# Optimization experiments

Hardware: AMD Instinct MI355X
Metric: run time of the kernel (lower is better)

## Reference

```python
import jax, jax.numpy as jnp
import numpy as np
from jax import lax

# ---- model dims (from init_kwargs) ----
H_SIZE = 2048      # hidden_size
NK = 16            # linear_num_key_heads
NV = 32            # linear_num_value_heads
DK = 128           # linear_key_head_dim
DV = 128           # linear_value_head_dim
KCONV = 4          # linear_conv_kernel_dim
KEY_DIM = NK * DK          # 2048
VAL_DIM = NV * DV          # 4096
CONV_DIM = 2 * KEY_DIM + VAL_DIM  # 8192
B, S = 2, 2048
EPS = 1e-6


def _l2norm(x, eps=EPS):
    return x * lax.rsqrt(jnp.sum(x * x, axis=-1, keepdims=True) + eps)


def setup_inputs() -> dict:
    key = jax.random.key(0)
    ks = jax.random.split(key, 7)
    x = jax.random.normal(ks[0], (B, S, H_SIZE), jnp.float32)
    W_qkvz = jax.random.normal(ks[1], (2 * KEY_DIM + 2 * VAL_DIM, H_SIZE), jnp.float32) * 0.02
    W_ba = jax.random.normal(ks[2], (2 * NV, H_SIZE), jnp.float32) * 0.02
    conv_w = jax.random.normal(ks[3], (CONV_DIM, 1, KCONV), jnp.float32) * 0.2  # depthwise OIH
    dt_bias = jnp.ones((NV,), jnp.float32)
    A_log = jnp.log(jax.random.uniform(ks[4], (NV,), jnp.float32, 1e-3, 16.0))
    norm_w = jnp.zeros((VAL_DIM,), jnp.float32)
    W_out = jax.random.normal(ks[5], (H_SIZE, VAL_DIM), jnp.float32) * 0.02
    return {"x": x, "W_qkvz": W_qkvz, "W_ba": W_ba, "conv_w": conv_w,
            "dt_bias": dt_bias, "A_log": A_log, "norm_w": norm_w, "W_out": W_out}


def reference(x, W_qkvz, W_ba, conv_w, dt_bias, A_log, norm_w, W_out):
    bs, s, _ = x.shape
    qkvz = jnp.einsum('bsh,ph->bsp', x, W_qkvz)
    ba = jnp.einsum('bsh,ph->bsp', x, W_ba)
    q, k, v, z = jnp.split(qkvz, [KEY_DIM, 2 * KEY_DIM, 2 * KEY_DIM + VAL_DIM], axis=-1)
    b, a = jnp.split(ba, [NV], axis=-1)

    # causal depthwise conv1d over channels (left pad K-1), then SiLU
    mixed = jnp.concatenate([q, k, v], axis=-1).transpose(0, 2, 1)  # [B, CONV_DIM, S]
    mixed = lax.conv_general_dilated(
        mixed, conv_w, window_strides=(1,), padding=[(KCONV - 1, 0)],
        dimension_numbers=('NCH', 'OIH', 'NCH'), feature_group_count=CONV_DIM)
    mixed = jax.nn.silu(mixed).transpose(0, 2, 1)  # [B, S, CONV_DIM]
    q, k, v = jnp.split(mixed, [KEY_DIM, 2 * KEY_DIM], axis=-1)

    q = q.reshape(bs, s, NK, DK)
    k = k.reshape(bs, s, NK, DK)
    v = v.reshape(bs, s, NV, DV)
    beta = jax.nn.sigmoid(b)                                   # [B,S,NV]
    g = -jnp.exp(A_log) * jax.nn.softplus(a + dt_bias)         # [B,S,NV]

    rep = NV // NK
    if rep > 1:
        q = jnp.repeat(q, rep, axis=2)
        k = jnp.repeat(k, rep, axis=2)
    q = _l2norm(q).astype(jnp.float32)
    k = _l2norm(k).astype(jnp.float32)
    v = v.astype(jnp.float32)

    # time-major for scan: [S, B, H, d]
    qs = q.transpose(1, 0, 2, 3)
    ks_ = k.transpose(1, 0, 2, 3)
    vs = v.transpose(1, 0, 2, 3)
    ge = jnp.exp(g).transpose(1, 0, 2)      # [S,B,H]
    bs_ = beta.astype(jnp.float32).transpose(1, 0, 2)  # [S,B,H]

    state0 = jnp.zeros((bs, NV, DK, DV), jnp.float32)

    def step(state, ts):
        q_t, k_t, v_t, g_t, b_t = ts
        state = state * g_t[..., None, None]
        kv_mem = jnp.einsum('bhk,bhkv->bhv', k_t, state)
        delta = b_t[..., None] * (v_t - kv_mem)
        state = state + jnp.einsum('bhk,bhv->bhkv', k_t, delta)
        o_t = jnp.einsum('bhk,bhkv->bhv', q_t, state)
        return state, o_t

    _, core = lax.scan(step, state0, (qs, ks_, vs, ge, bs_))  # core: [S,B,H,DV]
    core = core.transpose(1, 0, 2, 3).reshape(bs, s, VAL_DIM)

    # RMSNorm with (1 + weight) scale
    core = core * lax.rsqrt(jnp.mean(core * core, axis=-1, keepdims=True) + EPS)
    core = core * (1.0 + norm_w)
    core = core * jax.nn.silu(z)
    return jnp.einsum('bsv,hv->bsh', core, W_out)
```

## Files before the change

### kernel.cpp

```cpp
#include <hip/hip_runtime.h>
#include <hip/hip_bf16.h>
#include <math.h>

#define TOK    4096
#define HS     2048
#define CONVD  8192
#define KEYD   2048
#define VALD   4096
#define NKH    16
#define NVH    32
#define DKH    128
#define DVH    128
#define SEQ    2048
#define NBATCH 2
#define EPSF   1e-6f
#define CHUNK  64
#define NCHUNK 32

typedef __attribute__((ext_vector_type(8))) short short8;
typedef __attribute__((ext_vector_type(4))) float floatx4;

static __device__ __forceinline__ unsigned short f2bf(float x) {
  union { float f; unsigned u; } c; c.f = x;
  unsigned r = (c.u + 0x7FFF + ((c.u >> 16) & 1)) >> 16;
  return (unsigned short)r;
}
static __device__ __forceinline__ float bf2f(unsigned short u) {
  union { unsigned u; float f; } c; c.u = ((unsigned)u) << 16;
  return c.f;
}

#define BAR() do { \
  __builtin_amdgcn_sched_barrier(0); \
  asm volatile("s_waitcnt lgkmcnt(0)" ::: "memory"); \
  __builtin_amdgcn_s_barrier(); \
  __builtin_amdgcn_sched_barrier(0); \
} while (0)

__global__ __launch_bounds__(256) void gemm_nt(
    const float* __restrict__ A, const float* __restrict__ B,
    float* __restrict__ C, int M, int N, int K) {
  __shared__ float As[16][68];
  __shared__ float Bs[16][68];
  const int tx = threadIdx.x & 15;
  const int ty = threadIdx.x >> 4;
  const int row0 = blockIdx.y * 64;
  const int col0 = blockIdx.x * 64;
  const int lr = threadIdx.x >> 2;
  const int lc = (threadIdx.x & 3) * 4;
  float acc[4][4] = {};
  for (int k0 = 0; k0 < K; k0 += 16) {
    float4 av = *(const float4*)&A[(size_t)(row0 + lr) * K + (k0 + lc)];
    float4 bv = *(const float4*)&B[(size_t)(col0 + lr) * K + (k0 + lc)];
    As[lc + 0][lr] = av.x; As[lc + 1][lr] = av.y;
    As[lc + 2][lr] = av.z; As[lc + 3][lr] = av.w;
    Bs[lc + 0][lr] = bv.x; Bs[lc + 1][lr] = bv.y;
    Bs[lc + 2][lr] = bv.z; Bs[lc + 3][lr] = bv.w;
    __syncthreads();
    #pragma unroll
    for (int kk = 0; kk < 16; kk++) {
      float a[4], b[4];
      #pragma unroll
      for (int i = 0; i < 4; i++) a[i] = As[kk][ty * 4 + i];
      #pragma unroll
      for (int i = 0; i < 4; i++) b[i] = Bs[kk][tx * 4 + i];
      #pragma unroll
      for (int i = 0; i < 4; i++)
        #pragma unroll
        for (int j = 0; j < 4; j++)
          acc[i][j] += a[i] * b[j];
    }
    __syncthreads();
  }
  #pragma unroll
  for (int i = 0; i < 4; i++) {
    float4 v = make_float4(acc[i][0], acc[i][1], acc[i][2], acc[i][3]);
    *(float4*)&C[(size_t)(row0 + ty * 4 + i) * N + (col0 + tx * 4)] = v;
  }
}

__global__ __launch_bounds__(256) void cast_bf16(
    const float4* __restrict__ src, ushort4* __restrict__ dst, int n4) {
  int i = blockIdx.x * 256 + threadIdx.x;
  if (i < n4) {
    float4 v = src[i];
    ushort4 o;
    o.x = f2bf(v.x); o.y = f2bf(v.y); o.z = f2bf(v.z); o.w = f2bf(v.w);
    dst[i] = o;
  }
}

__global__ __launch_bounds__(256) void gemm_bf16_nt(
    const ushort* __restrict__ A, const ushort* __restrict__ B,
    float* __restrict__ C, int M, int N, int K) {
  __shared__ ushort Asm[128 * 32];
  __shared__ ushort Bsm[128 * 32];
  const int tid = threadIdx.x;
  const int w = tid >> 6, l = tid & 63;
  const int row0 = blockIdx.y * 128, col0 = blockIdx.x * 128;
  const int wm = w >> 1, wn = w & 1;

  floatx4 acc[4][4];
  #pragma unroll
  for (int i = 0; i < 4; i++)
    #pragma unroll
    for (int j = 0; j < 4; j++)
      acc[i][j] = (floatx4){0.f, 0.f, 0.f, 0.f};

  const int srow = w * 16 + (l >> 2);
  const int scol = (l & 3) * 8;
  const ushort* Ag = A + (size_t)(row0 + srow) * K + scol;
  const ushort* Bg = B + (size_t)(col0 + srow) * K + scol;

  for (int k0 = 0; k0 < K; k0 += 32) {
    #pragma unroll
    for (int c = 0; c < 2; c++) {
      __builtin_amdgcn_global_load_lds(
          (const __attribute__((address_space(1))) void*)(Ag + (size_t)(c * 64) * K + k0),
          (__attribute__((address_space(3))) void*)&Asm[(c * 64 + w * 16) * 32],
          16, 0, 0);
      __builtin_amdgcn_global_load_lds(
          (const __attribute__((address_space(1))) void*)(Bg + (size_t)(c * 64) * K + k0),
          (__attribute__((address_space(3))) void*)&Bsm[(c * 64 + w * 16) * 32],
          16, 0, 0);
    }
    __syncthreads();
    short8 af[4], bfv[4];
    #pragma unroll
    for (int i = 0; i < 4; i++) {
      af[i]  = *(const short8*)&Asm[(wm * 64 + i * 16 + (l & 15)) * 32 + (l >> 4) * 8];
      bfv[i] = *(const short8*)&Bsm[(wn * 64 + i * 16 + (l & 15)) * 32 + (l >> 4) * 8];
    }
    #pragma unroll
    for (int i = 0; i < 4; i++)
      #pragma unroll
      for (int j = 0; j < 4; j++)
        acc[i][j] = __builtin_amdgcn_mfma_f32_16x16x32_bf16(af[i], bfv[j], acc[i][j], 0, 0, 0);
    __syncthreads();
  }

  const int cl = l & 15, rq = l >> 4;
  #pragma unroll
  for (int i = 0; i < 4; i++) {
    int r0 = row0 + wm * 64 + i * 16 + rq * 4;
    #pragma unroll
    for (int j = 0; j < 4; j++) {
      int cc = col0 + wn * 64 + j * 16 + cl;
      #pragma unroll
      for (int r = 0; r < 4; r++)
        C[(size_t)(r0 + r) * N + cc] = acc[i][j][r];
    }
  }
}

__global__ __launch_bounds__(256) void conv_silu(
    const float* __restrict__ qkv, const float* __restrict__ cw,
    float* __restrict__ mix) {
  size_t idx = (size_t)blockIdx.x * 256 + threadIdx.x;
  int c = (int)(idx % CONVD);
  size_t t = idx / CONVD;
  int s = (int)(t % SEQ);
  float w0 = cw[c * 4 + 0], w1 = cw[c * 4 + 1], w2 = cw[c * 4 + 2], w3 = cw[c * 4 + 3];
  const float* col = qkv + t * CONVD + c;
  float acc = w3 * col[0];
  if (s >= 1) acc += w2 * col[-(ptrdiff_t)CONVD];
  if (s >= 2) acc += w1 * col[-2 * (ptrdiff_t)CONVD];
  if (s >= 3) acc += w0 * col[-3 * (ptrdiff_t)CONVD];
  float sig = 1.f / (1.f + expf(-acc));
  mix[t * CONVD + c] = acc * sig;
}

__global__ __launch_bounds__(256) void gates_kernel(
    const float* __restrict__ ba, const float* __restrict__ A_log,
    const float* __restrict__ dt_bias, float2* __restrict__ g2) {
  int idx = blockIdx.x * 256 + threadIdx.x;
  int h = idx & 31;
  size_t t = (size_t)(idx >> 5);
  float bv = ba[t * 64 + h];
  float av = ba[t * 64 + 32 + h];
  float beta = 1.f / (1.f + expf(-bv));
  float xx = av + dt_bias[h];
  float sp = (xx > 20.f) ? xx : log1pf(expf(xx));
  float lg = -expf(A_log[h]) * sp;
  g2[t * 32 + h] = make_float2(lg, beta);
}

__global__ __launch_bounds__(256) void l2norm_qk(
    const float* __restrict__ mix, ushort* __restrict__ kq) {
  int wid = (blockIdx.x * 256 + threadIdx.x) >> 6;
  int lane = threadIdx.x & 63;
  size_t t = (size_t)(wid >> 5);
  int hh = wid & 31;
  const float* p = mix + t * CONVD + (size_t)hh * DKH;
  float v0 = p[lane], v1 = p[lane + 64];
  float ss = v0 * v0 + v1 * v1;
  #pragma unroll
  for (int off = 32; off >= 1; off >>= 1) ss += __shfl_xor(ss, off, 64);
  float sc = rsqrtf(ss + EPSF);
  ushort* q = kq + t * 4096 + (size_t)hh * DKH;
  q[lane] = f2bf(v0 * sc);
  q[lane + 64] = f2bf(v1 * sc);
}

__global__ __launch_bounds__(64) void chunk_prep(
    const ushort* __restrict__ kq, const float2* __restrict__ g2,
    float* __restrict__ Lgbuf, ushort* __restrict__ Tbuf,
    ushort* __restrict__ Mbuf) {
  const int blk = blockIdx.x;
  const int ch = blk & 31;
  const int h  = (blk >> 5) & 31;
  const int b  = blk >> 10;
  const int kh = h >> 1;
  const int l  = threadIdx.x;
  const int fr = l & 15;
  const int fc8 = (l >> 4) * 8;
  const int cr = (l >> 4) * 4;

  __shared__ float sLg[64], sB[64];
  __shared__ float sA[64 * 65];
  __shared__ float sT[64 * 65];

  float2 gv = g2[((size_t)(b * SEQ + ch * 64 + l)) * 32 + h];
  float lg = gv.x;
  #pragma unroll
  for (int off = 1; off < 64; off <<= 1) {
    float n = __shfl_up(lg, off, 64);
    if (l >= off) lg += n;
  }
  sLg[l] = lg; sB[l] = gv.y;
  Lgbuf[(size_t)blk * 64 + l] = lg;
  __syncthreads();

  const ushort* qb = kq + ((size_t)(b * SEQ + ch * 64)) * 4096 + (size_t)kh * DKH;
  const ushort* kb = qb + 2048;

  floatx4 zero4 = {0.f, 0.f, 0.f, 0.f};
  floatx4 kk[4][4], qk[4][4];
  #pragma unroll
  for (int i = 0; i < 4; i++)
    #pragma unroll
    for (int j = 0; j < 4; j++) { kk[i][j] = zero4; qk[i][j] = zero4; }

  for (int ks = 0; ks < 4; ks++) {
    short8 kf[4], qf[4];
    #pragma unroll
    for (int m = 0; m < 4; m++) {
      kf[m] = *(const short8*)(kb + (size_t)(m * 16 + fr) * 4096 + fc8 + ks * 32);
      qf[m] = *(const short8*)(qb + (size_t)(m * 16 + fr) * 4096 + fc8 + ks * 32);
    }
    #pragma unroll
    for (int mt = 0; mt < 4; mt++)
      #pragma unroll
      for (int nt = 0; nt < 4; nt++) {
        kk[mt][nt] = __builtin_amdgcn_mfma_f32_16x16x32_bf16(kf[mt], kf[nt], kk[mt][nt], 0, 0, 0);
        qk[mt][nt] = __builtin_amdgcn_mfma_f32_16x16x32_bf16(qf[mt], kf[nt], qk[mt][nt], 0, 0, 0);
      }
  }

  const size_t tmbase = (size_t)blk * 4096;
  #pragma unroll
  for (int mt = 0; mt < 4; mt++)
    #pragma unroll
    for (int r = 0; r < 4; r++) {
      int i = mt * 16 + cr + r;
      float Li = sLg[i], Bi = sB[i];
      #pragma unroll
      for (int nt = 0; nt < 4; nt++) {
        int j = nt * 16 + fr;
        float dec = expf(Li - sLg[j]);
        sA[i * 65 + j] = (j < i) ? Bi * dec * kk[mt][nt][r] : 0.f;
        float mv = (j <= i) ? dec * qk[mt][nt][r] : 0.f;
        Mbuf[tmbase + (size_t)i * 64 + j] = f2bf(mv);
      }
    }
  __syncthreads();

  sT[0 * 65 + l] = (l == 0) ? 1.f : 0.f;
  for (int i = 1; i < 64; i++) {
    float acc = (l == i) ? 1.f : 0.f;
    for (int j = 0; j < i; j++)
      acc -= sA[i * 65 + j] * sT[j * 65 + l];
    sT[i * 65 + l] = acc;
  }
  for (int i = 0; i < 64; i++)
    Tbuf[tmbase + (size_t)i * 64 + l] = f2bf(sT[i * 65 + l]);
}

struct KReg { short8 K[4]; float gLg, gB, gLgC; };

__global__ __launch_bounds__(256, 1) void chunk_scan(
    const float* __restrict__ mix, const ushort* __restrict__ kq,
    const float2* __restrict__ g2, const float* __restrict__ Lgbuf,
    const ushort* __restrict__ Tbuf, const ushort* __restrict__ Mbuf,
    float* __restrict__ core) {
  const int blk = blockIdx.x;
  const int vq = blk & 3;
  const int bh = blk >> 2;
  const int h = bh & 31;
  const int b = bh >> 5;
  const int kh = h >> 1;
  const int tid = threadIdx.x;
  const int w = tid >> 6;
  const int l = tid & 63;
  const int fr = l & 15;
  const int fc8 = (l >> 4) * 8;
  const int cr = (l >> 4) * 4;
  const int w16 = w * 16, w32 = w * 32;
  const int ia = w16 + fr;

  __shared__ __align__(16) ushort Kt[64][136];
  __shared__ __align__(16) ushort STh[32][136], STl[32][136];
  __shared__ __align__(16) ushort DTh[32][72],  DTl[32][72];
  __shared__ float sKB[64], sQv[64], sKh[64], sBe[64], sLgC[1];

  for (int i = tid; i < 32 * 136; i += 256) { (&STh[0][0])[i] = 0; (&STl[0][0])[i] = 0; }

  floatx4 zero4 = {0.f, 0.f, 0.f, 0.f};
  floatx4 sacc[2][2] = {{zero4, zero4}, {zero4, zero4}};

  const size_t mixb = (size_t)b * SEQ * CONVD;
  const float* vb = mix + mixb + 2 * KEYD + (size_t)h * DVH + vq * 32;
  const ushort* kq_q = kq + (size_t)b * SEQ * 4096 + (size_t)kh * DKH;
  const ushort* kq_k = kq_q + 2048;
  const ushort* Tb = Tbuf + (size_t)bh * 32 * 4096;
  const ushort* Mb = Mbuf + (size_t)bh * 32 * 4096;
  const float* Lgb = Lgbuf + (size_t)bh * 2048;
  const float2* gp = g2 + (size_t)b * SEQ * 32 + h;
  float* cbase = core + (size_t)b * SEQ * VALD + (size_t)h * DVH + vq * 32;

  auto kpre = [&](KReg& R, int ch) {
    size_t ro = (size_t)(ch * 64 + ia) * 4096;
    #pragma unroll
    for (int ks = 0; ks < 4; ks++)
      R.K[ks] = *(const short8*)(kq_k + ro + fc8 + ks * 32);
    if (tid < 64) {
      R.gLg = Lgb[ch * 64 + tid];
      R.gLgC = Lgb[ch * 64 + 63];
      R.gB = gp[(size_t)(ch * 64 + tid) * 32].y;
    }
  };

  auto body = [&](KReg& cur, KReg& nxt, int ch) {
    const int tok0 = ch * 64;
    if (tid < 64) {
      float e = expf(cur.gLg);
      sKB[tid] = cur.gB * e;
      sQv[tid] = e;
      sKh[tid] = expf(cur.gLgC - cur.gLg);
      sBe[tid] = cur.gB;
      if (tid == 0) sLgC[0] = cur.gLgC;
    }
    #pragma unroll
    for (int ks = 0; ks < 4; ks++)
      *(short8*)&Kt[ia][fc8 + ks * 32] = cur.K[ks];
    short8 Qr[4], Tr[2], Mr[2];
    float Vr[8];
    {
      size_t ro = (size_t)(tok0 + ia) * 4096;
      #pragma unroll
      for (int ks = 0; ks < 4; ks++)
        Qr[ks] = *(const short8*)(kq_q + ro + fc8 + ks * 32);
      size_t tmb = (size_t)ch * 4096 + (size_t)ia * 64;
      #pragma unroll
      for (int ks = 0; ks < 2; ks++) {
        Tr[ks] = *(const short8*)(Tb + tmb + fc8 + ks * 32);
        Mr[ks] = *(const short8*)(Mb + tmb + fc8 + ks * 32);
      }
      #pragma unroll
      for (int nt = 0; nt < 2; nt++)
        #pragma unroll
        for (int r = 0; r < 4; r++)
          Vr[nt * 4 + r] = vb[(size_t)(tok0 + w16 + cr + r) * CONVD + nt * 16 + fr];
    }
    BAR();
    kpre(nxt, (ch + 1 < NCHUNK) ? ch + 1 : NCHUNK - 1);

    floatx4 p[2] = {zero4, zero4};
    #pragma unroll
    for (int ks = 0; ks < 4; ks++)
      #pragma unroll
      for (int nt = 0; nt < 2; nt++) {
        short8 bh_ = *(const short8*)&STh[nt * 16 + fr][fc8 + ks * 32];
        short8 bl_ = *(const short8*)&STl[nt * 16 + fr][fc8 + ks * 32];
        p[nt] = __builtin_amdgcn_mfma_f32_16x16x32_bf16(cur.K[ks], bh_, p[nt], 0, 0, 0);
        p[nt] = __builtin_amdgcn_mfma_f32_16x16x32_bf16(cur.K[ks], bl_, p[nt], 0, 0, 0);
      }
    #pragma unroll
    for (int nt = 0; nt < 2; nt++) {
      unsigned hv[4], lv[4];
      #pragma unroll
      for (int r = 0; r < 4; r++) {
        int i = w16 + cr + r;
        float Rv = sBe[i] * Vr[nt * 4 + r] - sKB[i] * p[nt][r];
        unsigned short hq = f2bf(Rv);
        hv[r] = hq; lv[r] = f2bf(Rv - bf2f(hq));
      }
      int v = nt * 16 + fr;
      *(uint2*)&DTh[v][w16 + cr] = make_uint2(hv[0] | (hv[1] << 16), hv[2] | (hv[3] << 16));
      *(uint2*)&DTl[v][w16 + cr] = make_uint2(lv[0] | (lv[1] << 16), lv[2] | (lv[3] << 16));
    }
    BAR();

    floatx4 d[2] = {zero4, zero4};
    #pragma unroll
    for (int ks = 0; ks < 2; ks++)
      #pragma unroll
      for (int nt = 0; nt < 2; nt++) {
        short8 bh_ = *(const short8*)&DTh[nt * 16 + fr][fc8 + ks * 32];
        short8 bl_ = *(const short8*)&DTl[nt * 16 + fr][fc8 + ks * 32];
        d[nt] = __builtin_amdgcn_mfma_f32_16x16x32_bf16(Tr[ks], bh_, d[nt], 0, 0, 0);
        d[nt] = __builtin_amdgcn_mfma_f32_16x16x32_bf16(Tr[ks], bl_, d[nt], 0, 0, 0);
      }
    BAR();
    #pragma unroll
    for (int nt = 0; nt < 2; nt++) {
      unsigned hv[4], lv[4];
      #pragma unroll
      for (int r = 0; r < 4; r++) {
        float dv = d[nt][r];
        unsigned short hq = f2bf(dv);
        hv[r] = hq; lv[r] = f2bf(dv - bf2f(hq));
      }
      int v = nt * 16 + fr;
      *(uint2*)&DTh[v][w16 + cr] = make_uint2(hv[0] | (hv[1] << 16), hv[2] | (hv[3] << 16));
      *(uint2*)&DTl[v][w16 + cr] = make_uint2(lv[0] | (lv[1] << 16), lv[2] | (lv[3] << 16));
    }
    BAR();

    floatx4 oq[2] = {zero4, zero4}, od[2] = {zero4, zero4};
    #pragma unroll
    for (int ks = 0; ks < 4; ks++)
      #pragma unroll
      for (int nt = 0; nt < 2; nt++) {
        short8 bh_ = *(const short8*)&STh[nt * 16 + fr][fc8 + ks * 32];
        short8 bl_ = *(const short8*)&STl[nt * 16 + fr][fc8 + ks * 32];
        oq[nt] = __builtin_amdgcn_mfma_f32_16x16x32_bf16(Qr[ks], bh_, oq[nt], 0, 0, 0);
        oq[nt] = __builtin_amdgcn_mfma_f32_16x16x32_bf16(Qr[ks], bl_, oq[nt], 0, 0, 0);
      }
    #pragma unroll
    for (int ks = 0; ks < 2; ks++)
      #pragma unroll
      for (int nt = 0; nt < 2; nt++) {
        short8 bh_ = *(const short8*)&DTh[nt * 16 + fr][fc8 + ks * 32];
        short8 bl_ = *(const short8*)&DTl[nt * 16 + fr][fc8 + ks * 32];
        od[nt] = __builtin_amdgcn_mfma_f32_16x16x32_bf16(Mr[ks], bh_, od[nt], 0, 0, 0);
        od[nt] = __builtin_amdgcn_mfma_f32_16x16x32_bf16(Mr[ks], bl_, od[nt], 0, 0, 0);
      }
    #pragma unroll
    for (int nt = 0; nt < 2; nt++)
      #pragma unroll
      for (int r = 0; r < 4; r++) {
        int i = w16 + cr + r;
        cbase[(size_t)(tok0 + i) * VALD + nt * 16 + fr] = sQv[i] * oq[nt][r] + od[nt][r];
      }

    float eL = expf(sLgC[0]);
    #pragma unroll
    for (int mt = 0; mt < 2; mt++)
      #pragma unroll
      for (int nt = 0; nt < 2; nt++)
        #pragma unroll
        for (int r = 0; r < 4; r++)
          sacc[mt][nt][r] *= eL;
    #pragma unroll
    for (int ks = 0; ks < 2; ks++) {
      short8 afm[2];
      #pragma unroll
      for (int mt = 0; mt < 2; mt++) {
        short8 a;
        #pragma unroll
        for (int jj = 0; jj < 8; jj++) {
          int tk = fc8 + ks * 32 + jj;
          float kv = bf2f(Kt[tk][w32 + mt * 16 + fr]);
          a[jj] = (short)f2bf(kv * sKh[tk]);
        }
        afm[mt] = a;
      }
      #pragma unroll
      for (int mt = 0; mt < 2; mt++)
        #pragma unroll
        for (int nt = 0; nt < 2; nt++) {
          short8 bh_ = *(const short8*)&DTh[nt * 16 + fr][fc8 + ks * 32];
          short8 bl_ = *(const short8*)&DTl[nt * 16 + fr][fc8 + ks * 32];
          sacc[mt][nt] = __builtin_amdgcn_mfma_f32_16x16x32_bf16(afm[mt], bh_, sacc[mt][nt], 0, 0, 0);
          sacc[mt][nt] = __builtin_amdgcn_mfma_f32_16x16x32_bf16(afm[mt], bl_, sacc[mt][nt], 0, 0, 0);
        }
    }
    BAR();
    #pragma unroll
    for (int mt = 0; mt < 2; mt++)
      #pragma unroll
      for (int nt = 0; nt < 2; nt++) {
        unsigned hv[4], lv[4];
        #pragma unroll
        for (int r = 0; r < 4; r++) {
          float sv = sacc[mt][nt][r];
          unsigned short hq = f2bf(sv);
          hv[r] = hq; lv[r] = f2bf(sv - bf2f(hq));
        }
        int v = nt * 16 + fr, k0 = w32 + mt * 16 + cr;
        *(uint2*)&STh[v][k0] = make_uint2(hv[0] | (hv[1] << 16), hv[2] | (hv[3] << 16));
        *(uint2*)&STl[v][k0] = make_uint2(lv[0] | (lv[1] << 16), lv[2] | (lv[3] << 16));
      }
  };

  KReg RA, RB;
  RA.gLg = RA.gB = RA.gLgC = 0.f;
  RB.gLg = RB.gB = RB.gLgC = 0.f;
  kpre(RA, 0);
  #pragma unroll 1
  for (int ch = 0; ch < NCHUNK; ch += 2) {
    body(RA, RB, ch);
    body(RB, RA, ch + 1);
  }
}

__global__ __launch_bounds__(256) void rmsnorm_silu(
    const float* __restrict__ core, const float* __restrict__ zbuf,
    const float* __restrict__ norm_w, ushort* __restrict__ out_bf) {
  int t = blockIdx.x;
  int tid = threadIdx.x;
  const float* row = core + (size_t)t * VALD;
  const float* zrow = zbuf + (size_t)t * VALD;
  ushort* orow = out_bf + (size_t)t * VALD;
  float vals[16];
  float ss = 0.f;
  #pragma unroll
  for (int i = 0; i < 16; i++) { float x = row[tid + i * 256]; vals[i] = x; ss += x * x; }
  #pragma unroll
  for (int off = 32; off >= 1; off >>= 1) ss += __shfl_xor(ss, off, 64);
  __shared__ float red[4];
  if ((tid & 63) == 0) red[tid >> 6] = ss;
  __syncthreads();
  float tot = red[0] + red[1] + red[2] + red[3];
  float scale = rsqrtf(tot * (1.f / VALD) + EPSF);
  #pragma unroll
  for (int i = 0; i < 16; i++) {
    int c = tid + i * 256;
    float z = zrow[c];
    float sz = z / (1.f + expf(-z));
    orow[c] = f2bf(vals[i] * scale * (1.f + norm_w[c]) * sz);
  }
}

extern "C" void kernel_launch(void* const* d_in, const int* in_sizes, int n_in,
                              void* d_out, int out_size, void* d_ws, size_t ws_size,
                              hipStream_t stream) {
  const float* x       = (const float*)d_in[0];
  const float* W_qkvz  = (const float*)d_in[1];
  const float* W_ba    = (const float*)d_in[2];
  const float* conv_w  = (const float*)d_in[3];
  const float* dt_bias = (const float*)d_in[4];
  const float* A_log   = (const float*)d_in[5];
  const float* norm_w  = (const float*)d_in[6];
  const float* W_out   = (const float*)d_in[7];
  float* out = (float*)d_out;

  float* ws = (float*)d_ws;
  float* A  = ws;
  float* Bp = A + (size_t)33554432;
  float* Cp = Bp + (size_t)33554432;
  float* ba = Cp + (size_t)16777216;
  float* g2 = ba + (size_t)262144;

  ushort* x_bf    = (ushort*)Cp;
  ushort* Wqkv_bf = (ushort*)Bp;
  float*  zb      = A;
  ushort* core_bf = (ushort*)(A + (size_t)16777216);
  ushort* Wz_bf   = (ushort*)(A + (size_t)25165824);
  ushort* Wo_bf   = (ushort*)Bp;
  float*  mix     = Bp;
  float*  core    = Cp;
  ushort* Tbuf    = (ushort*)(A + (size_t)16777216);
  ushort* Mbuf    = (ushort*)(A + (size_t)20971520);
  ushort* kq_bf   = (ushort*)(A + (size_t)25165824);
  float*  Lgbuf   = ba;

  cast_bf16<<<(TOK * HS / 4 + 255) / 256, 256, 0, stream>>>((const float4*)x, (ushort4*)x_bf, TOK * HS / 4);
  cast_bf16<<<(CONVD * HS / 4 + 255) / 256, 256, 0, stream>>>((const float4*)W_qkvz, (ushort4*)Wqkv_bf, CONVD * HS / 4);
  gemm_bf16_nt<<<dim3(CONVD / 128, TOK / 128), 256, 0, stream>>>(x_bf, Wqkv_bf, A, TOK, CONVD, HS);
  gemm_nt<<<dim3(1, TOK / 64), 256, 0, stream>>>(x, W_ba, ba, TOK, 64, HS);
  conv_silu<<<(int)(((size_t)TOK * CONVD) / 256), 256, 0, stream>>>(A, conv_w, mix);
  cast_bf16<<<(VALD * HS / 4 + 255) / 256, 256, 0, stream>>>(
      (const float4*)(W_qkvz + (size_t)(2 * KEYD + VALD) * HS), (ushort4*)Wz_bf, VALD * HS / 4);
  gemm_bf16_nt<<<dim3(VALD / 128, TOK / 128), 256, 0, stream>>>(x_bf, Wz_bf, zb, TOK, VALD, HS);
  gates_kernel<<<TOK * NVH / 256, 256, 0, stream>>>(ba, A_log, dt_bias, (float2*)g2);
  l2norm_qk<<<TOK * 32 / 4, 256, 0, stream>>>(mix, kq_bf);
  chunk_prep<<<NBATCH * NVH * NCHUNK, 64, 0, stream>>>(kq_bf, (const float2*)g2, Lgbuf, Tbuf, Mbuf);
  chunk_scan<<<NBATCH * NVH * 4, 256, 0, stream>>>(mix, kq_bf, (const float2*)g2, Lgbuf, Tbuf, Mbuf, core);
  rmsnorm_silu<<<TOK, 256, 0, stream>>>(core, zb, norm_w, core_bf);
  cast_bf16<<<(HS * VALD / 4 + 255) / 256, 256, 0, stream>>>((const float4*)W_out, (ushort4*)Wo_bf, HS * VALD / 4);
  gemm_bf16_nt<<<dim3(HS / 128, TOK / 128), 256, 0, stream>>>(core_bf, Wo_bf, out, TOK, HS, VALD);
}
```

Baseline: 1.106 ms.

## Replace bf16 GEMM with 256x256 double-buffered, swizzled, pipelined MFMA kernel

Swaps the 128x128 tile, single-buffered bf16 GEMM for a 256x256 tile kernel with 512 threads and BK=64. Global-to-LDS loads are double-buffered and staged in quarter pieces interleaved with the MFMA phases. LDS rows are XOR-swizzled to avoid bank conflicts, and s_setprio and sched barriers control issue order. The aim is to hide memory latency and raise arithmetic intensity in the three projection GEMMs, at the cost of more LDS (128KB) and registers, and fewer blocks for the smaller GEMMs (the output GEMM has only 128 blocks).

```diff
diff --git a/kernel.cpp b/kernel.cpp
--- a/kernel.cpp
+++ b/kernel.cpp
@@ -90,62 +90,171 @@
   }
 }
 
-__global__ __launch_bounds__(256) void gemm_bf16_nt(
+#define GBM 256
+#define GBK 64
+
+#define STAGE(DST, SRC, BUF, HALF, KT) do { \
+  __builtin_amdgcn_global_load_lds( \
+      (const __attribute__((address_space(1))) void*)((SRC) + (size_t)((HALF) * 128) * K + (size_t)(KT) * 64), \
+      (__attribute__((address_space(3))) void*)&DST[BUF][((HALF) * 128 + wrow) * GBK], 16, 0, 0); \
+  __builtin_amdgcn_global_load_lds( \
+      (const __attribute__((address_space(1))) void*)((SRC) + (size_t)((HALF) * 128 + 64) * K + (size_t)(KT) * 64), \
+      (__attribute__((address_space(3))) void*)&DST[BUF][((HALF) * 128 + 64 + wrow) * GBK], 16, 0, 0); \
+} while (0)
+
+__global__ __launch_bounds__(512, 2) void gemm256(
     const ushort* __restrict__ A, const ushort* __restrict__ B,
     float* __restrict__ C, int M, int N, int K) {
-  __shared__ ushort Asm[128 * 32];
-  __shared__ ushort Bsm[128 * 32];
+  __shared__ ushort As[2][GBM * GBK];
+  __shared__ ushort Bs[2][GBM * GBK];
+
   const int tid = threadIdx.x;
   const int w = tid >> 6, l = tid & 63;
-  const int row0 = blockIdx.y * 128, col0 = blockIdx.x * 128;
-  const int wm = w >> 1, wn = w & 1;
-
-  floatx4 acc[4][4];
-  #pragma unroll
-  for (int i = 0; i < 4; i++)
+  const int wm = w >> 2, wn = w & 3;
+  const int row0 = blockIdx.y * GBM, col0 = blockIdx.x * GBM;
+  const int nt = K >> 6;
+
+  const int srow = tid >> 3;
+  const int sunit = (tid & 7) ^ (srow & 7);
+  const int wrow = w * 8;
+  const ushort* Ag = A + (size_t)(row0 + srow) * K + sunit * 8;
+  const ushort* Bg = B + (size_t)(col0 + srow) * K + sunit * 8;
+
+  const int aoff = (wm * 128 + (l & 15)) * GBK;
+  const int boff = (wn * 64 + (l & 15)) * GBK;
+  const int u0 = (((l >> 4) ^ (l & 7)) * 8);
+  const int u1 = u0 ^ 32;
+
+  floatx4 acc[8][4];
+  #pragma unroll
+  for (int i = 0; i < 8; i++)
     #pragma unroll
     for (int j = 0; j < 4; j++)
       acc[i][j] = (floatx4){0.f, 0.f, 0.f, 0.f};
 
-  const int srow = w * 16 + (l >> 2);
-  const int scol = (l & 3) * 8;
-  const ushort* Ag = A + (size_t)(row0 + srow) * K + scol;
-  const ushort* Bg = B + (size_t)(col0 + srow) * K + scol;
-
-  for (int k0 = 0; k0 < K; k0 += 32) {
-    #pragma unroll
-    for (int c = 0; c < 2; c++) {
-      __builtin_amdgcn_global_load_lds(
-          (const __attribute__((address_space(1))) void*)(Ag + (size_t)(c * 64) * K + k0),
-          (__attribute__((address_space(3))) void*)&Asm[(c * 64 + w * 16) * 32],
-          16, 0, 0);
-      __builtin_amdgcn_global_load_lds(
-          (const __attribute__((address_space(1))) void*)(Bg + (size_t)(c * 64) * K + k0),
-          (__attribute__((address_space(3))) void*)&Bsm[(c * 64 + w * 16) * 32],
-          16, 0, 0);
-    }
-    __syncthreads();
-    short8 af[4], bfv[4];
-    #pragma unroll
-    for (int i = 0; i < 4; i++) {
-      af[i]  = *(const short8*)&Asm[(wm * 64 + i * 16 + (l & 15)) * 32 + (l >> 4) * 8];
-      bfv[i] = *(const short8*)&Bsm[(wn * 64 + i * 16 + (l & 15)) * 32 + (l >> 4) * 8];
-    }
-    #pragma unroll
-    for (int i = 0; i < 4; i++)
-      #pragma unroll
-      for (int j = 0; j < 4; j++)
-        acc[i][j] = __builtin_amdgcn_mfma_f32_16x16x32_bf16(af[i], bfv[j], acc[i][j], 0, 0, 0);
-    __syncthreads();
+  STAGE(Bs, Bg, 0, 0, 0);
+  STAGE(As, Ag, 0, 0, 0);
+  STAGE(As, Ag, 0, 1, 0);
+  STAGE(Bs, Bg, 0, 1, 0);
+  STAGE(Bs, Bg, 1, 0, 1);
+  STAGE(As, Ag, 1, 0, 1);
+  asm volatile("s_waitcnt vmcnt(4)" ::: "memory");
+  __builtin_amdgcn_sched_barrier(0);
+  __builtin_amdgcn_s_barrier();
+  __builtin_amdgcn_sched_barrier(0);
+
+  short8 rA[4][2], rB0[2][2], rB1[2][2];
+
+  #pragma unroll 1
+  for (int t = 0; t < nt; ++t) {
+    const int buf = t & 1, nbuf = buf ^ 1;
+    const ushort* Ab = &As[buf][0];
+    const ushort* Bb = &Bs[buf][0];
+
+    #pragma unroll
+    for (int fm = 0; fm < 4; fm++) {
+      rA[fm][0] = *(const short8*)&Ab[aoff + (fm * 16) * GBK + u0];
+      rA[fm][1] = *(const short8*)&Ab[aoff + (fm * 16) * GBK + u1];
+    }
+    #pragma unroll
+    for (int fn = 0; fn < 2; fn++) {
+      rB0[fn][0] = *(const short8*)&Bb[boff + (fn * 16) * GBK + u0];
+      rB0[fn][1] = *(const short8*)&Bb[boff + (fn * 16) * GBK + u1];
+    }
+    if (t + 1 < nt) STAGE(As, Ag, nbuf, 1, t + 1);
+    __builtin_amdgcn_sched_barrier(0);
+    __builtin_amdgcn_s_barrier();
+    asm volatile("s_waitcnt lgkmcnt(0)" ::: "memory");
+    __builtin_amdgcn_sched_barrier(0);
+    __builtin_amdgcn_s_setprio(1);
+    #pragma unroll
+    for (int ks = 0; ks < 2; ks++)
+      #pragma unroll
+      for (int fm = 0; fm < 4; fm++)
+        #pragma unroll
+        for (int fn = 0; fn < 2; fn++)
+          acc[fm][fn] = __builtin_amdgcn_mfma_f32_16x16x32_bf16(rA[fm][ks], rB0[fn][ks], acc[fm][fn], 0, 0, 0);
+    __builtin_amdgcn_s_setprio(0);
+    __builtin_amdgcn_sched_barrier(0);
+    __builtin_amdgcn_s_barrier();
+    __builtin_amdgcn_sched_barrier(0);
+
+    #pragma unroll
+    for (int fn = 0; fn < 2; fn++) {
+      rB1[fn][0] = *(const short8*)&Bb[boff + (32 + fn * 16) * GBK + u0];
+      rB1[fn][1] = *(const short8*)&Bb[boff + (32 + fn * 16) * GBK + u1];
+    }
+    if (t + 1 < nt) STAGE(Bs, Bg, nbuf, 1, t + 1);
+    __builtin_amdgcn_sched_barrier(0);
+    __builtin_amdgcn_s_barrier();
+    asm volatile("s_waitcnt lgkmcnt(0)" ::: "memory");
+    __builtin_amdgcn_sched_barrier(0);
+    __builtin_amdgcn_s_setprio(1);
+    #pragma unroll
+    for (int ks = 0; ks < 2; ks++)
+      #pragma unroll
+      for (int fm = 0; fm < 4; fm++)
+        #pragma unroll
+        for (int fn = 0; fn < 2; fn++)
+          acc[fm][2 + fn] = __builtin_amdgcn_mfma_f32_16x16x32_bf16(rA[fm][ks], rB1[fn][ks], acc[fm][2 + fn], 0, 0, 0);
+    __builtin_amdgcn_s_setprio(0);
+    __builtin_amdgcn_sched_barrier(0);
+    __builtin_amdgcn_s_barrier();
+    __builtin_amdgcn_sched_barrier(0);
+
+    #pragma unroll
+    for (int fm = 0; fm < 4; fm++) {
+      rA[fm][0] = *(const short8*)&Ab[aoff + (64 + fm * 16) * GBK + u0];
+      rA[fm][1] = *(const short8*)&Ab[aoff + (64 + fm * 16) * GBK + u1];
+    }
+    if (t + 2 < nt) STAGE(Bs, Bg, buf, 0, t + 2);
+    __builtin_amdgcn_sched_barrier(0);
+    __builtin_amdgcn_s_barrier();
+    asm volatile("s_waitcnt lgkmcnt(0)" ::: "memory");
+    __builtin_amdgcn_sched_barrier(0);
+    __builtin_amdgcn_s_setprio(1);
+    #pragma unroll
+    for (int ks = 0; ks < 2; ks++)
+      #pragma unroll
+      for (int fm = 0; fm < 4; fm++)
+        #pragma unroll
+        for (int fn = 0; fn < 2; fn++)
+          acc[4 + fm][2 + fn] = __builtin_amdgcn_mfma_f32_16x16x32_bf16(rA[fm][ks], rB1[fn][ks], acc[4 + fm][2 + fn], 0, 0, 0);
+    __builtin_amdgcn_s_setprio(0);
+    __builtin_amdgcn_sched_barrier(0);
+    __builtin_amdgcn_s_barrier();
+    __builtin_amdgcn_sched_barrier(0);
+
+    if (t + 2 < nt) STAGE(As, Ag, buf, 0, t + 2);
+    __builtin_amdgcn_sched_barrier(0);
+    __builtin_amdgcn_s_barrier();
+    __builtin_amdgcn_sched_barrier(0);
+    __builtin_amdgcn_s_setprio(1);
+    #pragma unroll
+    for (int ks = 0; ks < 2; ks++)
+      #pragma unroll
+      for (int fm = 0; fm < 4; fm++)
+        #pragma unroll
+        for (int fn = 0; fn < 2; fn++)
+          acc[4 + fm][fn] = __builtin_amdgcn_mfma_f32_16x16x32_bf16(rA[fm][ks], rB0[fn][ks], acc[4 + fm][fn], 0, 0, 0);
+    __builtin_amdgcn_s_setprio(0);
+    if (t + 2 < nt) {
+      asm volatile("s_waitcnt vmcnt(4)" ::: "memory");
+    } else if (t + 1 < nt) {
+      asm volatile("s_waitcnt vmcnt(0)" ::: "memory");
+    }
+    __builtin_amdgcn_sched_barrier(0);
+    __builtin_amdgcn_s_barrier();
+    __builtin_amdgcn_sched_barrier(0);
   }
 
   const int cl = l & 15, rq = l >> 4;
   #pragma unroll
-  for (int i = 0; i < 4; i++) {
-    int r0 = row0 + wm * 64 + i * 16 + rq * 4;
+  for (int i = 0; i < 8; i++) {
+    int r0 = row0 + wm * 128 + (i >> 2) * 64 + (i & 3) * 16 + rq * 4;
     #pragma unroll
     for (int j = 0; j < 4; j++) {
-      int cc = col0 + wn * 64 + j * 16 + cl;
+      int cc = col0 + wn * 64 + (j >> 1) * 32 + (j & 1) * 16 + cl;
       #pragma unroll
       for (int r = 0; r < 4; r++)
         C[(size_t)(r0 + r) * N + cc] = acc[i][j][r];
@@ -578,17 +687,17 @@
 
   cast_bf16<<<(TOK * HS / 4 + 255) / 256, 256, 0, stream>>>((const float4*)x, (ushort4*)x_bf, TOK * HS / 4);
   cast_bf16<<<(CONVD * HS / 4 + 255) / 256, 256, 0, stream>>>((const float4*)W_qkvz, (ushort4*)Wqkv_bf, CONVD * HS / 4);
-  gemm_bf16_nt<<<dim3(CONVD / 128, TOK / 128), 256, 0, stream>>>(x_bf, Wqkv_bf, A, TOK, CONVD, HS);
+  gemm256<<<dim3(CONVD / 256, TOK / 256), 512, 0, stream>>>(x_bf, Wqkv_bf, A, TOK, CONVD, HS);
   gemm_nt<<<dim3(1, TOK / 64), 256, 0, stream>>>(x, W_ba, ba, TOK, 64, HS);
   conv_silu<<<(int)(((size_t)TOK * CONVD) / 256), 256, 0, stream>>>(A, conv_w, mix);
   cast_bf16<<<(VALD * HS / 4 + 255) / 256, 256, 0, stream>>>(
       (const float4*)(W_qkvz + (size_t)(2 * KEYD + VALD) * HS), (ushort4*)Wz_bf, VALD * HS / 4);
-  gemm_bf16_nt<<<dim3(VALD / 128, TOK / 128), 256, 0, stream>>>(x_bf, Wz_bf, zb, TOK, VALD, HS);
+  gemm256<<<dim3(VALD / 256, TOK / 256), 512, 0, stream>>>(x_bf, Wz_bf, zb, TOK, VALD, HS);
   gates_kernel<<<TOK * NVH / 256, 256, 0, stream>>>(ba, A_log, dt_bias, (float2*)g2);
   l2norm_qk<<<TOK * 32 / 4, 256, 0, stream>>>(mix, kq_bf);
   chunk_prep<<<NBATCH * NVH * NCHUNK, 64, 0, stream>>>(kq_bf, (const float2*)g2, Lgbuf, Tbuf, Mbuf);
   chunk_scan<<<NBATCH * NVH * 4, 256, 0, stream>>>(mix, kq_bf, (const float2*)g2, Lgbuf, Tbuf, Mbuf, core);
   rmsnorm_silu<<<TOK, 256, 0, stream>>>(core, zb, norm_w, core_bf);
   cast_bf16<<<(HS * VALD / 4 + 255) / 256, 256, 0, stream>>>((const float4*)W_out, (ushort4*)Wo_bf, HS * VALD / 4);
-  gemm_bf16_nt<<<dim3(HS / 128, TOK / 128), 256, 0, stream>>>(core_bf, Wo_bf, out, TOK, HS, VALD);
-}
+  gemm256<<<dim3(HS / 256, TOK / 256), 512, 0, stream>>>(core_bf, Wo_bf, out, TOK, HS, VALD);
+}
```

New measurement: 1.037 ms. 1.07x faster.
